# Kernel optimization log

Hardware: AMD Instinct MI355X
Metric: run time of the kernel (lower is better)

## Reference

```python
import jax, jax.numpy as jnp
import numpy as np

H = 256            # hidden_size
N_NODE = 50000     # item vocab
NUM_GRAPHS = 4096
NODES_PER_G = 20
EDGES_PER_G = 40
N = NUM_GRAPHS * NODES_PER_G      # 81920
E = NUM_GRAPHS * EDGES_PER_G      # 163840


def setup_inputs() -> dict:
    key = jax.random.key(0)
    ks = jax.random.split(key, 16)
    stdv = 1.0 / np.sqrt(H)
    u = lambda k, shape: jax.random.uniform(k, shape, jnp.float32, -stdv, stdv)

    # graph data: 1-based item ids, sorted batch vector, within-graph edges
    x = jax.random.randint(ks[0], (N,), 1, N_NODE, dtype=jnp.int64)
    batch = jnp.repeat(jnp.arange(NUM_GRAPHS, dtype=jnp.int64), NODES_PER_G)
    base = jnp.repeat(jnp.arange(NUM_GRAPHS, dtype=jnp.int64) * NODES_PER_G, EDGES_PER_G)
    src = base + jax.random.randint(ks[1], (E,), 0, NODES_PER_G, dtype=jnp.int64)
    dst = base + jax.random.randint(ks[2], (E,), 0, NODES_PER_G, dtype=jnp.int64)
    edge_index = jnp.stack([src, dst])

    return {
        "x": x, "edge_index": edge_index, "batch": batch,
        "emb": u(ks[3], (N_NODE, H)),
        "gated_w": u(ks[4], (2, H, H)),      # GatedGraphConv weight, num_layers=2
        "w_ih": u(ks[5], (3 * H, H)), "w_hh": u(ks[6], (3 * H, H)),
        "b_ih": u(ks[7], (3 * H,)), "b_hh": u(ks[8], (3 * H,)),
        "W1": u(ks[9], (H, H)), "b1": u(ks[10], (H,)),
        "W2": u(ks[11], (H, H)), "b2": u(ks[12], (H,)),
        "qw": u(ks[13], (1, H)), "qb": u(ks[14], (1,)),
        "W3": u(ks[15], (H, 2 * H)), "b3": jnp.zeros((H,), jnp.float32),
    }


def _forward(x, edge_index, batch, emb, gated_w, w_ih, w_hh, b_ih, b_hh,
             W1, b1, W2, b2, qw, qb, W3, b3):
    h = emb[x - 1]                                   # [N, H] embedding lookup
    src, dst = edge_index[0], edge_index[1]

    # GatedGraphConv: 2 layers of (linear -> scatter-add over edges -> GRUCell)
    for i in range(2):
        m = h @ gated_w[i]                           # [N, H]
        agg = jnp.zeros_like(h).at[dst].add(m[src])  # message aggregation
        gi = agg @ w_ih.T + b_ih                     # GRU input gates
        gh = h @ w_hh.T + b_hh                       # GRU hidden gates
        i_r, i_z, i_n = jnp.split(gi, 3, axis=-1)
        h_r, h_z, h_n = jnp.split(gh, 3, axis=-1)
        r = jax.nn.sigmoid(i_r + h_r)
        z = jax.nn.sigmoid(i_z + h_z)
        n = jnp.tanh(i_n + r * h_n)
        h = (1.0 - z) * n + z * h

    # Embedding2Score: last-node attention readout per graph
    counts = jnp.bincount(batch, length=NUM_GRAPHS)          # [B]
    last_idx = jnp.cumsum(counts) - 1                        # last node of each graph
    v_n = h[last_idx]                                        # [B, H]
    alpha = jax.nn.sigmoid(v_n[batch] @ W1.T + b1 + h @ W2.T + b2) @ qw.T + qb  # [N, 1]
    s_g = jax.ops.segment_sum(alpha * h, batch, num_segments=NUM_GRAPHS)        # [B, H]
    s_h = jnp.concatenate([v_n, s_g], axis=-1) @ W3.T + b3                      # [B, H]
    return s_h @ emb.T                                       # [B, N_NODE] scores


def reference(x, edge_index, batch, emb, gated_w, w_ih, w_hh, b_ih, b_hh,
              W1, b1, W2, b2, qw, qb, W3, b3):
    return _forward(x, edge_index, batch, emb, gated_w, w_ih, w_hh, b_ih, b_hh,
                    W1, b1, W2, b2, qw, qb, W3, b3)
```

## Files before the change

kernel.cpp:

```cpp
#include <hip/hip_runtime.h>

typedef __attribute__((ext_vector_type(8))) __bf16 bf16x8;
typedef __attribute__((ext_vector_type(4))) float f32x4;

#define DEV __device__ __forceinline__

DEV unsigned short f2bf(float f) {
  unsigned u = __float_as_uint(f);
  u = (u + 0x7fffu + ((u >> 16) & 1u)) >> 16;
  return (unsigned short)u;
}
DEV float bf2f(unsigned short s) { return __uint_as_float(((unsigned)s) << 16); }
DEV float sigm(float x) { return 1.f / (1.f + expf(-x)); }

DEV uint4 pack8(f32x4 a, f32x4 b) {
  uint4 o;
  o.x = (unsigned)f2bf(a[0]) | ((unsigned)f2bf(a[1]) << 16);
  o.y = (unsigned)f2bf(a[2]) | ((unsigned)f2bf(a[3]) << 16);
  o.z = (unsigned)f2bf(b[0]) | ((unsigned)f2bf(b[1]) << 16);
  o.w = (unsigned)f2bf(b[2]) | ((unsigned)f2bf(b[3]) << 16);
  return o;
}

#define GL16(SRC, LDSB)                                                                    \
  __builtin_amdgcn_global_load_lds(                                                       \
      (const __attribute__((address_space(1))) unsigned int*)(SRC),                       \
      (__attribute__((address_space(3))) unsigned int*)(LDSB), 16, 0, 0)

template<int MODE, bool BIAS>
__global__ __launch_bounds__(256)
void gemm_bt(const unsigned short* __restrict__ A, const unsigned short* __restrict__ Bm,
             const float* __restrict__ bias, void* __restrict__ Cv,
             const float* __restrict__ vw1, const float* __restrict__ qwf,
             const int* __restrict__ batchp, int M, int N, int K)
{
  __shared__ unsigned short sm[16384];
  unsigned short* As = sm;
  unsigned short* Bs = sm + 8192;

  const int tid  = threadIdx.x;
  const int lane = tid & 63;
  const int wv   = tid >> 6;
  const int wr   = (wv >> 1) << 6;
  const int wc   = (wv & 1) << 6;
  const long mTile = (long)blockIdx.y << 7;
  const long nTile = (long)blockIdx.x << 7;

  const f32x4 z4 = {0.f, 0.f, 0.f, 0.f};
  f32x4 acc[4][4];
  #pragma unroll
  for (int i = 0; i < 4; ++i)
    #pragma unroll
    for (int j = 0; j < 4; ++j) acc[i][j] = z4;

  const int crow = lane >> 3;
  const int ckb  = (lane & 7) << 4;

  for (int k0 = 0; k0 < K; k0 += 64) {
    #pragma unroll
    for (int i = 0; i < 4; ++i) {
      const int c   = (wv << 2) + i;
      const int row = (c << 3) + crow;
      const int kb  = ckb ^ ((row & 7) << 4);
      const unsigned short* sA = A + (mTile + row) * K + k0 + (kb >> 1);
      GL16(sA, (char*)As + (c << 10));
      int bn = (int)nTile + row; bn = bn < N ? bn : (N - 1);
      const unsigned short* sB = Bm + (long)bn * K + k0 + (kb >> 1);
      GL16(sB, (char*)Bs + (c << 10));
    }
    __syncthreads();
    #pragma unroll
    for (int kk = 0; kk < 64; kk += 32) {
      const int kbl = (kk + ((lane >> 4) << 3)) << 1;
      bf16x8 af[4], bfv[4];
      #pragma unroll
      for (int mi = 0; mi < 4; ++mi) {
        const int rr = wr + (mi << 4) + (lane & 15);
        af[mi] = *(const bf16x8*)((const char*)As + (rr << 7) + (kbl ^ ((rr & 7) << 4)));
      }
      #pragma unroll
      for (int ni = 0; ni < 4; ++ni) {
        const int rr = wc + (ni << 4) + (lane & 15);
        bfv[ni] = *(const bf16x8*)((const char*)Bs + (rr << 7) + (kbl ^ ((rr & 7) << 4)));
      }
      #pragma unroll
      for (int mi = 0; mi < 4; ++mi)
        #pragma unroll
        for (int ni = 0; ni < 4; ++ni)
          acc[mi][ni] = __builtin_amdgcn_mfma_f32_16x16x32_bf16(af[mi], bfv[ni], acc[mi][ni], 0, 0, 0);
    }
    __syncthreads();
  }

  if constexpr (MODE == 2) {
    const int slice = (int)blockIdx.x * 2 + (wc >> 6);
    #pragma unroll
    for (int mi = 0; mi < 4; ++mi) {
      #pragma unroll
      for (int j = 0; j < 4; ++j) {
        const long row = mTile + wr + (mi << 4) + ((lane >> 4) << 2) + j;
        const long vb = (long)batchp[row] << 8;
        float part = 0.f;
        #pragma unroll
        for (int ni = 0; ni < 4; ++ni) {
          const int col = (int)nTile + wc + (ni << 4) + (lane & 15);
          part += sigm(acc[mi][ni][j] + vw1[vb + col]) * qwf[col];
        }
        #pragma unroll
        for (int off = 1; off < 16; off <<= 1) part += __shfl_xor(part, off, 64);
        if ((lane & 15) == 0) ((float*)Cv)[(long)slice * M + row] = part;
      }
    }
  } else {
    #pragma unroll
    for (int ni = 0; ni < 4; ++ni) {
      const long col = nTile + wc + (ni << 4) + (lane & 15);
      if (col < N) {
        float bv = 0.f;
        if constexpr (BIAS) bv = bias[col];
        #pragma unroll
        for (int mi = 0; mi < 4; ++mi) {
          const long row = mTile + wr + (mi << 4) + ((lane >> 4) << 2);
          #pragma unroll
          for (int j = 0; j < 4; ++j) {
            const float v = acc[mi][ni][j] + bv;
            if constexpr (MODE == 1) ((unsigned short*)Cv)[(row + j) * N + col] = f2bf(v);
            else                     ((float*)Cv)[(row + j) * N + col] = v;
          }
        }
      }
    }
  }
}

__global__ __launch_bounds__(512, 2)
void k_ggru(const unsigned short* __restrict__ agg, const unsigned short* __restrict__ hin,
            const unsigned short* __restrict__ wihb, const unsigned short* __restrict__ whhb,
            const float* __restrict__ bih, const float* __restrict__ bhh,
            unsigned short* __restrict__ hout)
{
  extern __shared__ unsigned short sm[];
  const int tid  = threadIdx.x;
  const int lane = tid & 63;
  const int wv   = tid >> 6;
  const int rh   = wv >> 2;
  const int cg   = wv & 3;
  const int D0   = blockIdx.x << 6;
  const long mTile = (long)blockIdx.y << 7;

  const f32x4 z4 = {0.f, 0.f, 0.f, 0.f};
  f32x4 acc[4][6];
  #pragma unroll
  for (int i = 0; i < 4; ++i)
    #pragma unroll
    for (int g = 0; g < 6; ++g) acc[i][g] = z4;

  const int crow = lane >> 3;
  const int ckb  = (lane & 7) << 4;

  for (int k0 = 0; k0 < 256; k0 += 64) {
    #pragma unroll
    for (int i = 0; i < 10; ++i) {
      const int c = wv * 10 + i;
      if (c < 32) {
        const unsigned short* src = (c < 16) ? agg : hin;
        const int row = ((c & 15) << 3) + crow;
        const int kb  = ckb ^ ((row & 7) << 4);
        GL16(src + (mTile + row) * 256 + k0 + (kb >> 1), (char*)sm + (c << 10));
      } else {
        const int g  = (c - 32) >> 3;
        const int lr = (((c - 32) & 7) << 3) + crow;
        const unsigned short* Ws = (g < 3) ? wihb : whhb;
        const long grow = (long)((g % 3) * 256 + D0 + lr);
        const int kb = ckb ^ ((lr & 7) << 4);
        GL16(Ws + grow * 256 + k0 + (kb >> 1), (char*)sm + (c << 10));
      }
    }
    __syncthreads();
    #pragma unroll
    for (int kk = 0; kk < 64; kk += 32) {
      const int kbl = (kk + ((lane >> 4) << 3)) << 1;
      bf16x8 fa[4], fh[4], fb[6];
      #pragma unroll
      for (int mi = 0; mi < 4; ++mi) {
        const int r = (rh << 6) + (mi << 4) + (lane & 15);
        const int off = (r << 7) + (kbl ^ ((r & 7) << 4));
        fa[mi] = *(const bf16x8*)((const char*)sm + off);
        fh[mi] = *(const bf16x8*)((const char*)sm + 16384 + off);
      }
      const int lr = (cg << 4) + (lane & 15);
      const int boff = (lr << 7) + (kbl ^ ((lr & 7) << 4));
      #pragma unroll
      for (int g = 0; g < 6; ++g)
        fb[g] = *(const bf16x8*)((const char*)sm + 32768 + (g << 13) + boff);
      #pragma unroll
      for (int mi = 0; mi < 4; ++mi) {
        #pragma unroll
        for (int g = 0; g < 3; ++g)
          acc[mi][g] = __builtin_amdgcn_mfma_f32_16x16x32_bf16(fa[mi], fb[g], acc[mi][g], 0, 0, 0);
        #pragma unroll
        for (int g = 3; g < 6; ++g)
          acc[mi][g] = __builtin_amdgcn_mfma_f32_16x16x32_bf16(fh[mi], fb[g], acc[mi][g], 0, 0, 0);
      }
    }
    __syncthreads();
  }

  const int d = D0 + (cg << 4) + (lane & 15);
  const float bir = bih[d], biz = bih[256 + d], bin_ = bih[512 + d];
  const float bhr = bhh[d], bhz = bhh[256 + d], bhn  = bhh[512 + d];
  #pragma unroll
  for (int mi = 0; mi < 4; ++mi) {
    #pragma unroll
    for (int j = 0; j < 4; ++j) {
      const long row = mTile + (rh << 6) + (mi << 4) + ((lane >> 4) << 2) + j;
      const float hold = bf2f(hin[row * 256 + d]);
      const float r  = sigm(acc[mi][0][j] + bir + acc[mi][3][j] + bhr);
      const float z  = sigm(acc[mi][1][j] + biz + acc[mi][4][j] + bhz);
      const float n  = tanhf(acc[mi][2][j] + bin_ + r * (acc[mi][5][j] + bhn));
      hout[row * 256 + d] = f2bf((1.f - z) * n + z * hold);
    }
  }
}

__global__ void k_pre(const int* __restrict__ x, const float* __restrict__ emb,
                      unsigned short* __restrict__ embb, unsigned short* __restrict__ h,
                      const float* __restrict__ wih, const float* __restrict__ whh,
                      const float* __restrict__ W1, const float* __restrict__ W2,
                      const float* __restrict__ W3, const float* __restrict__ b1,
                      const float* __restrict__ b2, const float* __restrict__ gw,
                      unsigned short* __restrict__ wihb, unsigned short* __restrict__ whhb,
                      unsigned short* __restrict__ w1b, unsigned short* __restrict__ w2b,
                      unsigned short* __restrict__ w3b, float* __restrict__ b12,
                      unsigned short* __restrict__ gtw, int V8, int Nn8)
{
  const int b = blockIdx.x, t = threadIdx.x;
  if (b < V8) {
    const long i = (long)b * 256 + t;
    const f32x4 a = *(const f32x4*)(emb + i * 8);
    const f32x4 c = *(const f32x4*)(emb + i * 8 + 4);
    *(uint4*)(embb + i * 8) = pack8(a, c);
  } else if (b < V8 + Nn8) {
    const long i = (long)(b - V8) * 256 + t;
    const long node = i >> 5;
    const int  d0 = ((int)i & 31) << 3;
    const long row = (long)x[node] - 1;
    const float* p = emb + row * 256 + d0;
    const f32x4 a = *(const f32x4*)p;
    const f32x4 c = *(const f32x4*)(p + 4);
    *(uint4*)(h + node * 256 + d0) = pack8(a, c);
  } else {
    const int bw = b - V8 - Nn8;
    if (bw < 256) {
      const float* src; unsigned short* dst; int base;
      if (bw < 96)       { src = wih; dst = wihb; base = bw; }
      else if (bw < 192) { src = whh; dst = whhb; base = bw - 96; }
      else if (bw < 224) { src = W1;  dst = w1b;  base = bw - 192; }
      else               { src = W2;  dst = w2b;  base = bw - 224; }
      const long i = (long)base * 256 + t;
      const f32x4 a = *(const f32x4*)(src + i * 8);
      const f32x4 c = *(const f32x4*)(src + i * 8 + 4);
      *(uint4*)(dst + i * 8) = pack8(a, c);
    } else if (bw < 320) {
      const long i = (long)(bw - 256) * 256 + t;
      const f32x4 a = *(const f32x4*)(W3 + i * 8);
      const f32x4 c = *(const f32x4*)(W3 + i * 8 + 4);
      *(uint4*)(w3b + i * 8) = pack8(a, c);
    } else if (bw == 320) {
      b12[t] = b1[t] + b2[t];
    } else {
      const int bb = bw - 321;
      const int mat = bb >> 8, n = bb & 255;
      gtw[mat * 65536 + n * 256 + t] = f2bf(gw[mat * 65536 + t * 256 + n]);
    }
  }
}

__global__ void k_scatter(const unsigned short* __restrict__ m, const int* __restrict__ ei,
                          unsigned short* __restrict__ agg, int E)
{
  __shared__ float aggs[20 * 256];
  __shared__ int es[40], ed[40];
  const int g = blockIdx.x;
  const int d = threadIdx.x;
  if (d < 40) es[d] = ei[g * 40 + d];
  if (d >= 128 && d < 168) ed[d - 128] = ei[E + g * 40 + (d - 128)];
  #pragma unroll
  for (int i = 0; i < 20; ++i) aggs[i * 256 + d] = 0.f;
  __syncthreads();
  for (int e = 0; e < 40; ++e) {
    const float mv = bf2f(m[(long)es[e] * 256 + d]);
    const int loc = ed[e] - g * 20;
    aggs[loc * 256 + d] += mv;
  }
  const long base = (long)g * (20 * 256);
  #pragma unroll
  for (int i = 0; i < 20; ++i)
    agg[base + i * 256 + d] = f2bf(aggs[i * 256 + d]);
}

__global__ void k_vn(const unsigned short* __restrict__ h, const int* __restrict__ batch,
                     unsigned short* __restrict__ vn, unsigned short* __restrict__ cat, int n)
{
  const long i = (long)blockIdx.x * 256 + threadIdx.x;
  const long g = i >> 5;
  const int  d0 = ((int)i & 31) << 3;
  int lo = 0, hi = n;
  while (lo < hi) { const int mid = (lo + hi) >> 1; if (batch[mid] > (int)g) hi = mid; else lo = mid + 1; }
  const uint4 v = *(const uint4*)(h + (long)(lo - 1) * 256 + d0);
  *(uint4*)(vn + g * 256 + d0) = v;
  *(uint4*)(cat + g * 512 + d0) = v;
}

__global__ void k_sg(const float* __restrict__ alph2, const float* __restrict__ qb,
                     const unsigned short* __restrict__ h, unsigned short* __restrict__ cat, int Nn)
{
  __shared__ float al[20];
  const int g = blockIdx.x, d = threadIdx.x;
  if (d < 20) {
    const int n = g * 20 + d;
    al[d] = qb[0] + alph2[n] + alph2[Nn + n] + alph2[2 * Nn + n] + alph2[3 * Nn + n];
  }
  __syncthreads();
  float s = 0.f;
  const unsigned short* hp = h + (long)g * 20 * 256 + d;
  #pragma unroll
  for (int i = 0; i < 20; ++i) s += al[i] * bf2f(hp[i * 256]);
  cat[(long)g * 512 + 256 + d] = f2bf(s);
}

extern "C" void kernel_launch(void* const* d_in, const int* in_sizes, int n_in,
                              void* d_out, int out_size, void* d_ws, size_t ws_size,
                              hipStream_t stream)
{
  const int*   x     = (const int*)  d_in[0];
  const int*   ei    = (const int*)  d_in[1];
  const int*   batch = (const int*)  d_in[2];
  const float* emb   = (const float*)d_in[3];
  const float* gw    = (const float*)d_in[4];
  const float* wih   = (const float*)d_in[5];
  const float* whh   = (const float*)d_in[6];
  const float* bih   = (const float*)d_in[7];
  const float* bhh   = (const float*)d_in[8];
  const float* W1    = (const float*)d_in[9];
  const float* b1    = (const float*)d_in[10];
  const float* W2    = (const float*)d_in[11];
  const float* b2    = (const float*)d_in[12];
  const float* qw    = (const float*)d_in[13];
  const float* qb    = (const float*)d_in[14];
  const float* W3    = (const float*)d_in[15];
  const float* b3    = (const float*)d_in[16];

  const int Nn = in_sizes[0];
  const int E  = in_sizes[1] / 2;
  const int V  = in_sizes[3] / 256;
  const int B  = out_size / V;

  char* w = (char*)d_ws;
  auto take = [&](size_t bytes) { char* r = w; w += (bytes + 1023) & ~(size_t)1023; return r; };
  unsigned short* h_   = (unsigned short*)take((size_t)Nn * 256 * 2);
  unsigned short* m_   = (unsigned short*)take((size_t)Nn * 256 * 2);
  unsigned short* agg_ = (unsigned short*)take((size_t)Nn * 256 * 2);
  unsigned short* embb = (unsigned short*)take((size_t)V * 256 * 2);
  unsigned short* gtw  = (unsigned short*)take((size_t)2 * 65536 * 2);
  unsigned short* wihb = (unsigned short*)take((size_t)768 * 256 * 2);
  unsigned short* whhb = (unsigned short*)take((size_t)768 * 256 * 2);
  unsigned short* w1b  = (unsigned short*)take((size_t)65536 * 2);
  unsigned short* w2b  = (unsigned short*)take((size_t)65536 * 2);
  unsigned short* w3b  = (unsigned short*)take((size_t)131072 * 2);
  unsigned short* vnb  = (unsigned short*)take((size_t)B * 256 * 2);
  unsigned short* catb = (unsigned short*)take((size_t)B * 512 * 2);
  unsigned short* shb  = (unsigned short*)take((size_t)B * 256 * 2);
  float*          b12  = (float*)take(256 * 4);
  float*          alph2= (float*)take((size_t)4 * Nn * 4);
  float*          vw1  = (float*)take((size_t)B * 256 * 4);

  const int MBn = Nn / 128;
  const int MBb = B / 128;
  const int NBv = (V + 127) / 128;
  const int V8  = V / 8;
  const int Nn8 = Nn / 8;

  k_pre<<<dim3(V8 + Nn8 + 833), 256, 0, stream>>>(x, emb, embb, h_,
      wih, whh, W1, W2, W3, b1, b2, gw, wihb, whhb, w1b, w2b, w3b, b12, gtw, V8, Nn8);

  unsigned short* hc = h_;
  unsigned short* mb = m_;
  for (int L = 0; L < 2; ++L) {
    gemm_bt<1, false><<<dim3(2, MBn), 256, 0, stream>>>(hc, gtw + (size_t)L * 65536, nullptr, mb,
                                                        nullptr, nullptr, nullptr, Nn, 256, 256);
    k_scatter<<<dim3(B), 256, 0, stream>>>(mb, ei, agg_, E);
    k_ggru<<<dim3(4, MBn), 512, 81920, stream>>>(agg_, hc, wihb, whhb, bih, bhh, mb);
    unsigned short* t = hc; hc = mb; mb = t;
  }

  k_vn<<<dim3(B * 32 / 256), 256, 0, stream>>>(hc, batch, vnb, catb, Nn);
  gemm_bt<0, true><<<dim3(2, MBb), 256, 0, stream>>>(vnb, w1b, b12, vw1,
                                                     nullptr, nullptr, nullptr, B, 256, 256);
  gemm_bt<2, false><<<dim3(2, MBn), 256, 0, stream>>>(hc, w2b, nullptr, alph2,
                                                      vw1, qw, batch, Nn, 256, 256);
  k_sg<<<dim3(B), 256, 0, stream>>>(alph2, qb, hc, catb, Nn);
  gemm_bt<1, true><<<dim3(2, MBb), 256, 0, stream>>>(catb, w3b, b3, shb,
                                                     nullptr, nullptr, nullptr, B, 256, 512);

  gemm_bt<0, false><<<dim3(NBv, MBb), 256, 0, stream>>>(shb, embb, nullptr, (float*)d_out,
                                                        nullptr, nullptr, nullptr, B, V, 256);

  (void)n_in; (void)ws_size;
}
```

Measured before the change: 809.4 us.

## Fold gated conv weight into GRU input weights, scatter hidden state directly

Uses linearity of scatter-add: (A h) G W_ih^T = A h (W_ih G^T)... precomputes per-layer product wp = W_ih · G^T via small GEMMs, and scatters h directly instead of m = h@G. This removes the per-layer N×256×256 GEMM and its intermediate write/read. Adds two tiny 768×256 GEMMs and changes bf16 rounding order (product weight rounded to bf16).

New measurement: 761.2 us. 1.06x faster.

```diff
diff --git a/kernel.cpp b/kernel.cpp
--- a/kernel.cpp
+++ b/kernel.cpp
@@ -135,7 +135,7 @@
 
 __global__ __launch_bounds__(512, 2)
 void k_ggru(const unsigned short* __restrict__ agg, const unsigned short* __restrict__ hin,
-            const unsigned short* __restrict__ wihb, const unsigned short* __restrict__ whhb,
+            const unsigned short* __restrict__ wpb, const unsigned short* __restrict__ whhb,
             const float* __restrict__ bih, const float* __restrict__ bhh,
             unsigned short* __restrict__ hout)
 {
@@ -170,7 +170,7 @@
       } else {
         const int g  = (c - 32) >> 3;
         const int lr = (((c - 32) & 7) << 3) + crow;
-        const unsigned short* Ws = (g < 3) ? wihb : whhb;
+        const unsigned short* Ws = (g < 3) ? wpb : whhb;
         const long grow = (long)((g % 3) * 256 + D0 + lr);
         const int kb = ckb ^ ((lr & 7) << 4);
         GL16(Ws + grow * 256 + k0 + (kb >> 1), (char*)sm + (c << 10));
@@ -232,7 +232,7 @@
                       unsigned short* __restrict__ wihb, unsigned short* __restrict__ whhb,
                       unsigned short* __restrict__ w1b, unsigned short* __restrict__ w2b,
                       unsigned short* __restrict__ w3b, float* __restrict__ b12,
-                      unsigned short* __restrict__ gtw, int V8, int Nn8)
+                      unsigned short* __restrict__ gwb, int V8, int Nn8)
 {
   const int b = blockIdx.x, t = threadIdx.x;
   if (b < V8) {
@@ -251,28 +251,18 @@
     *(uint4*)(h + node * 256 + d0) = pack8(a, c);
   } else {
     const int bw = b - V8 - Nn8;
-    if (bw < 256) {
-      const float* src; unsigned short* dst; int base;
-      if (bw < 96)       { src = wih; dst = wihb; base = bw; }
-      else if (bw < 192) { src = whh; dst = whhb; base = bw - 96; }
-      else if (bw < 224) { src = W1;  dst = w1b;  base = bw - 192; }
-      else               { src = W2;  dst = w2b;  base = bw - 224; }
-      const long i = (long)base * 256 + t;
-      const f32x4 a = *(const f32x4*)(src + i * 8);
-      const f32x4 c = *(const f32x4*)(src + i * 8 + 4);
-      *(uint4*)(dst + i * 8) = pack8(a, c);
-    } else if (bw < 320) {
-      const long i = (long)(bw - 256) * 256 + t;
-      const f32x4 a = *(const f32x4*)(W3 + i * 8);
-      const f32x4 c = *(const f32x4*)(W3 + i * 8 + 4);
-      *(uint4*)(w3b + i * 8) = pack8(a, c);
-    } else if (bw == 320) {
-      b12[t] = b1[t] + b2[t];
-    } else {
-      const int bb = bw - 321;
-      const int mat = bb >> 8, n = bb & 255;
-      gtw[mat * 65536 + n * 256 + t] = f2bf(gw[mat * 65536 + t * 256 + n]);
-    }
+    const float* src; unsigned short* dst; long base;
+    if (bw < 96)       { src = wih; dst = wihb; base = bw; }
+    else if (bw < 192) { src = whh; dst = whhb; base = bw - 96; }
+    else if (bw < 224) { src = W1;  dst = w1b;  base = bw - 192; }
+    else if (bw < 256) { src = W2;  dst = w2b;  base = bw - 224; }
+    else if (bw < 320) { src = W3;  dst = w3b;  base = bw - 256; }
+    else if (bw == 320) { b12[t] = b1[t] + b2[t]; return; }
+    else               { src = gw;  dst = gwb;  base = bw - 321; }
+    const long i = base * 256 + t;
+    const f32x4 a = *(const f32x4*)(src + i * 8);
+    const f32x4 c = *(const f32x4*)(src + i * 8 + 4);
+    *(uint4*)(dst + i * 8) = pack8(a, c);
   }
 }
 
@@ -362,9 +352,11 @@
   unsigned short* m_   = (unsigned short*)take((size_t)Nn * 256 * 2);
   unsigned short* agg_ = (unsigned short*)take((size_t)Nn * 256 * 2);
   unsigned short* embb = (unsigned short*)take((size_t)V * 256 * 2);
-  unsigned short* gtw  = (unsigned short*)take((size_t)2 * 65536 * 2);
+  unsigned short* gwb  = (unsigned short*)take((size_t)2 * 65536 * 2);
   unsigned short* wihb = (unsigned short*)take((size_t)768 * 256 * 2);
   unsigned short* whhb = (unsigned short*)take((size_t)768 * 256 * 2);
+  unsigned short* wp0  = (unsigned short*)take((size_t)768 * 256 * 2);
+  unsigned short* wp1  = (unsigned short*)take((size_t)768 * 256 * 2);
   unsigned short* w1b  = (unsigned short*)take((size_t)65536 * 2);
   unsigned short* w2b  = (unsigned short*)take((size_t)65536 * 2);
   unsigned short* w3b  = (unsigned short*)take((size_t)131072 * 2);
@@ -381,16 +373,20 @@
   const int V8  = V / 8;
   const int Nn8 = Nn / 8;
 
-  k_pre<<<dim3(V8 + Nn8 + 833), 256, 0, stream>>>(x, emb, embb, h_,
-      wih, whh, W1, W2, W3, b1, b2, gw, wihb, whhb, w1b, w2b, w3b, b12, gtw, V8, Nn8);
+  k_pre<<<dim3(V8 + Nn8 + 385), 256, 0, stream>>>(x, emb, embb, h_,
+      wih, whh, W1, W2, W3, b1, b2, gw, wihb, whhb, w1b, w2b, w3b, b12, gwb, V8, Nn8);
+
+  gemm_bt<1, false><<<dim3(2, 6), 256, 0, stream>>>(wihb, gwb, nullptr, wp0,
+                                                    nullptr, nullptr, nullptr, 768, 256, 256);
+  gemm_bt<1, false><<<dim3(2, 6), 256, 0, stream>>>(wihb, gwb + 65536, nullptr, wp1,
+                                                    nullptr, nullptr, nullptr, 768, 256, 256);
 
   unsigned short* hc = h_;
   unsigned short* mb = m_;
   for (int L = 0; L < 2; ++L) {
-    gemm_bt<1, false><<<dim3(2, MBn), 256, 0, stream>>>(hc, gtw + (size_t)L * 65536, nullptr, mb,
-                                                        nullptr, nullptr, nullptr, Nn, 256, 256);
-    k_scatter<<<dim3(B), 256, 0, stream>>>(mb, ei, agg_, E);
-    k_ggru<<<dim3(4, MBn), 512, 81920, stream>>>(agg_, hc, wihb, whhb, bih, bhh, mb);
+    k_scatter<<<dim3(B), 256, 0, stream>>>(hc, ei, agg_, E);
+    k_ggru<<<dim3(4, MBn), 512, 81920, stream>>>(agg_, hc, (L == 0 ? wp0 : wp1), whhb,
+                                                 bih, bhh, mb);
     unsigned short* t = hc; hc = mb; mb = t;
   }
 
```
